# Performance work log

Hardware: AMD Instinct MI355X
Metric: run time of the kernel (lower is better)

The kernel has to match this reference:

```python
import jax, jax.numpy as jnp
import numpy as np

O_FEATURES = 4096
I_FEATURES = 4096
N_TOKENS = 8192


def _unpack_int4(packed, out_shape):
    # packed: int32 holding uint8 byte values; two signed int4 per byte (offset-8)
    p = packed.astype(jnp.int32)
    even = (p & 15) - 8          # low nibble
    odd = ((p >> 4) & 15) - 8    # high nibble
    # interleave: stacked[0::2] = even, stacked[1::2] = odd
    stacked = jnp.stack([even, odd], axis=-1).reshape(-1)
    return stacked.reshape(out_shape)


def setup_inputs() -> dict:
    key = jax.random.key(0)
    k1, k2, k3 = jax.random.split(key, 3)
    x = jax.random.normal(k1, (N_TOKENS, I_FEATURES), dtype=jnp.float32)
    packed_w = jax.random.randint(k2, (O_FEATURES * I_FEATURES // 2,), 0, 256, dtype=jnp.int32)
    # per-output-channel scale (positive, as produced by abs-max / qmax)
    scale = jax.random.uniform(k3, (O_FEATURES, 1), dtype=jnp.float32) * 0.01 + 1e-4
    return {"x": x, "packed_w": packed_w, "scale": scale}


def reference(x, packed_w, scale):
    # dequantize: unpack int4 -> target dtype, multiply per-row scale
    int_w = _unpack_int4(packed_w, (O_FEATURES, I_FEATURES)).astype(x.dtype)  # [O, I]
    w = int_w * scale.astype(x.dtype)  # scale broadcasts [O,1] over [O,I]
    # downstream quantized linear: y = x @ W^T
    return jnp.einsum('ni,oi->no', x, w)
```

## Files before the change

kernel.cpp:

```cpp
#include <hip/hip_runtime.h>

typedef unsigned char u8;
typedef signed char s8;
typedef unsigned int u32;
typedef __attribute__((ext_vector_type(4))) int i32x4;

#define M_TOK 8192
#define N_OUT 4096
#define K_IN  4096
#define NT    32

static __device__ __forceinline__ u32 pack4(float4 v, float inv) {
    int q0 = __float2int_rn(v.x * inv) & 255;
    int q1 = __float2int_rn(v.y * inv) & 255;
    int q2 = __float2int_rn(v.z * inv) & 255;
    int q3 = __float2int_rn(v.w * inv) & 255;
    return (u32)q0 | ((u32)q1 << 8) | ((u32)q2 << 16) | ((u32)q3 << 24);
}

__global__ __launch_bounds__(256) void quant_x_kernel(const float* __restrict__ x,
                                                      s8* __restrict__ xq,
                                                      float* __restrict__ sx) {
    int row = blockIdx.x;
    int t = threadIdx.x;
    const float4* xr = (const float4*)(x + (size_t)row * K_IN);
    float4 v0 = xr[t], v1 = xr[t + 256], v2 = xr[t + 512], v3 = xr[t + 768];
    float am = 0.f;
    am = fmaxf(am, fmaxf(fmaxf(fabsf(v0.x), fabsf(v0.y)), fmaxf(fabsf(v0.z), fabsf(v0.w))));
    am = fmaxf(am, fmaxf(fmaxf(fabsf(v1.x), fabsf(v1.y)), fmaxf(fabsf(v1.z), fabsf(v1.w))));
    am = fmaxf(am, fmaxf(fmaxf(fabsf(v2.x), fabsf(v2.y)), fmaxf(fabsf(v2.z), fabsf(v2.w))));
    am = fmaxf(am, fmaxf(fmaxf(fabsf(v3.x), fabsf(v3.y)), fmaxf(fabsf(v3.z), fabsf(v3.w))));
#pragma unroll
    for (int o = 32; o > 0; o >>= 1) am = fmaxf(am, __shfl_xor(am, o));
    __shared__ float red[4];
    if ((t & 63) == 0) red[t >> 6] = am;
    __syncthreads();
    am = fmaxf(fmaxf(red[0], red[1]), fmaxf(red[2], red[3]));
    float inv = (am > 0.f) ? 127.f / am : 0.f;
    if (t == 0) sx[row] = (am > 0.f) ? am / 127.f : 0.f;
    u32* out = (u32*)(xq + (size_t)row * K_IN);
    out[t]       = pack4(v0, inv);
    out[t + 256] = pack4(v1, inv);
    out[t + 512] = pack4(v2, inv);
    out[t + 768] = pack4(v3, inv);
}

__global__ __launch_bounds__(256) void unpack_w_kernel(const int* __restrict__ pw,
                                                       s8* __restrict__ wq, int n4) {
    int idx = blockIdx.x * blockDim.x + threadIdx.x;
    int stride = gridDim.x * blockDim.x;
    for (int i = idx; i < n4; i += stride) {
        int4 p = *(const int4*)(pw + (size_t)i * 4);
        u32 lo = (u32)(((p.x & 15) - 8) & 255)
               | ((u32)((((p.x >> 4) & 15) - 8) & 255) << 8)
               | ((u32)((((p.y) & 15) - 8) & 255) << 16)
               | ((u32)((((p.y >> 4) & 15) - 8) & 255) << 24);
        u32 hi = (u32)(((p.z & 15) - 8) & 255)
               | ((u32)((((p.z >> 4) & 15) - 8) & 255) << 8)
               | ((u32)((((p.w) & 15) - 8) & 255) << 16)
               | ((u32)((((p.w >> 4) & 15) - 8) & 255) << 24);
        uint2 o; o.x = lo; o.y = hi;
        *(uint2*)(wq + (size_t)i * 8) = o;
    }
}

#define MFMA(a, b, c) __builtin_amdgcn_mfma_i32_16x16x64_i8(a, b, c, 0, 0, 0)

static __device__ __forceinline__ i32x4 ldsv(const u8* p, int idx) {
    return *(const i32x4*)(p + idx);
}

#define MFMA16(A00, A01, A10, A11, M0, M1)                \
    acc[M0][0] = MFMA(A00, b00, acc[M0][0]);              \
    acc[M0][1] = MFMA(A00, b10, acc[M0][1]);              \
    acc[M0][2] = MFMA(A00, b20, acc[M0][2]);              \
    acc[M0][3] = MFMA(A00, b30, acc[M0][3]);              \
    acc[M1][0] = MFMA(A10, b00, acc[M1][0]);              \
    acc[M1][1] = MFMA(A10, b10, acc[M1][1]);              \
    acc[M1][2] = MFMA(A10, b20, acc[M1][2]);              \
    acc[M1][3] = MFMA(A10, b30, acc[M1][3]);              \
    acc[M0][0] = MFMA(A01, b01, acc[M0][0]);              \
    acc[M0][1] = MFMA(A01, b11, acc[M0][1]);              \
    acc[M0][2] = MFMA(A01, b21, acc[M0][2]);              \
    acc[M0][3] = MFMA(A01, b31, acc[M0][3]);              \
    acc[M1][0] = MFMA(A11, b01, acc[M1][0]);              \
    acc[M1][1] = MFMA(A11, b11, acc[M1][1]);              \
    acc[M1][2] = MFMA(A11, b21, acc[M1][2]);              \
    acc[M1][3] = MFMA(A11, b31, acc[M1][3]);

__global__ __launch_bounds__(512, 2) void gemm8p_i8_kernel(const s8* __restrict__ A,
                                                           const s8* __restrict__ B,
                                                           const float* __restrict__ sx,
                                                           const float* __restrict__ scale,
                                                           float* __restrict__ C) {
    __shared__ __align__(16) u8 lds[131072];

#define GLo(src, dstIdx)                                                        \
    __builtin_amdgcn_global_load_lds(                                           \
        (const __attribute__((address_space(1))) void*)(src),                   \
        (__attribute__((address_space(3))) void*)&lds[dstIdx], 16, 0, 0)

    int wg = blockIdx.x;
    int swz = (wg & 7) * 64 + (wg >> 3);
    int bm = swz >> 4;
    int bn = swz & 15;

    int t = threadIdx.x;
    int l = t & 63;
    int wid = t >> 6;
    int wr = wid >> 2;
    int wc = wid & 3;

    const size_t soff = (size_t)(t >> 3) * K_IN + (size_t)((((t & 7) ^ ((t >> 3) & 7)) << 4));
    const size_t S64 = (size_t)64 * K_IN;
    const int t16 = t * 16;

    const s8* Alo = A + (size_t)(bm * 256) * K_IN;
    const s8* Ahi = Alo + (size_t)128 * K_IN;
    const s8* Blo = B + (size_t)(bn * 256) * K_IN;
    const s8* Bhi = Blo + (size_t)128 * K_IN;

    const int kx = (l & 7) << 4;
    const int koff0 = (((l >> 4) << 4)) ^ kx;
    const int koff1 = koff0 ^ 64;
    const int aB = wr * 16384 + (l & 15) * 128;
    const int bB = 32768 + wc * 8192 + (l & 15) * 128;

    i32x4 acc[8][4] = {};

    GLo(Blo + soff, 32768 + t16);         GLo(Blo + soff + S64, 32768 + t16 + 8192);
    GLo(Bhi + soff, 49152 + t16);         GLo(Bhi + soff + S64, 49152 + t16 + 8192);
    GLo(Alo + soff, t16);                 GLo(Alo + soff + S64, t16 + 8192);
    GLo(Ahi + soff, 16384 + t16);         GLo(Ahi + soff + S64, 16384 + t16 + 8192);
    GLo(Blo + soff + 128, 98304 + t16);   GLo(Blo + soff + S64 + 128, 98304 + t16 + 8192);
    GLo(Bhi + soff + 128, 114688 + t16);  GLo(Bhi + soff + S64 + 128, 114688 + t16 + 8192);
    asm volatile("s_waitcnt vmcnt(4)" ::: "memory");
    __builtin_amdgcn_s_barrier();

    for (int T = 0; T < NT; ++T) {
        const int buf = T & 1;
        const u8* L = lds + buf * 65536;

        i32x4 b00 = ldsv(L, bB + koff0),        b01 = ldsv(L, bB + koff1);
        i32x4 b10 = ldsv(L, bB + 2048 + koff0), b11 = ldsv(L, bB + 2048 + koff1);
        i32x4 b20 = ldsv(L, bB + 4096 + koff0), b21 = ldsv(L, bB + 4096 + koff1);
        i32x4 b30 = ldsv(L, bB + 6144 + koff0), b31 = ldsv(L, bB + 6144 + koff1);
        i32x4 a00 = ldsv(L, aB + koff0),        a01 = ldsv(L, aB + koff1);
        i32x4 a10 = ldsv(L, aB + 2048 + koff0), a11 = ldsv(L, aB + 2048 + koff1);
        if (T + 1 < NT) {
            size_t ko = (size_t)(T + 1) * 128;
            int d = (buf ^ 1) * 65536 + t16;
            GLo(Alo + soff + ko, d);                 GLo(Alo + soff + S64 + ko, d + 8192);
            GLo(Ahi + soff + ko, d + 16384);         GLo(Ahi + soff + S64 + ko, d + 24576);
        }
        __builtin_amdgcn_s_barrier();
        asm volatile("s_waitcnt lgkmcnt(0)" ::: "memory");
        __builtin_amdgcn_s_setprio(1);
        MFMA16(a00, a01, a10, a11, 0, 1);
        __builtin_amdgcn_s_setprio(0);
        __builtin_amdgcn_s_barrier();

        a00 = ldsv(L, aB + 4096 + koff0); a01 = ldsv(L, aB + 4096 + koff1);
        a10 = ldsv(L, aB + 6144 + koff0); a11 = ldsv(L, aB + 6144 + koff1);
        if (T + 2 < NT) {
            size_t ko = (size_t)(T + 2) * 128;
            int d = buf * 65536 + 32768 + t16;
            GLo(Blo + soff + ko, d);  GLo(Blo + soff + S64 + ko, d + 8192);
        }
        __builtin_amdgcn_s_barrier();
        asm volatile("s_waitcnt lgkmcnt(0)" ::: "memory");
        __builtin_amdgcn_s_setprio(1);
        MFMA16(a00, a01, a10, a11, 2, 3);
        __builtin_amdgcn_s_setprio(0);
        __builtin_amdgcn_s_barrier();

        a00 = ldsv(L, aB + 8192 + koff0);  a01 = ldsv(L, aB + 8192 + koff1);
        a10 = ldsv(L, aB + 10240 + koff0); a11 = ldsv(L, aB + 10240 + koff1);
        if (T + 2 < NT) {
            size_t ko = (size_t)(T + 2) * 128;
            int d = buf * 65536 + 49152 + t16;
            GLo(Bhi + soff + ko, d);  GLo(Bhi + soff + S64 + ko, d + 8192);
        }
        __builtin_amdgcn_s_barrier();
        asm volatile("s_waitcnt lgkmcnt(0)" ::: "memory");
        __builtin_amdgcn_s_setprio(1);
        MFMA16(a00, a01, a10, a11, 4, 5);
        __builtin_amdgcn_s_setprio(0);
        __builtin_amdgcn_s_barrier();

        a00 = ldsv(L, aB + 12288 + koff0); a01 = ldsv(L, aB + 12288 + koff1);
        a10 = ldsv(L, aB + 14336 + koff0); a11 = ldsv(L, aB + 14336 + koff1);
        __builtin_amdgcn_s_barrier();
        asm volatile("s_waitcnt lgkmcnt(0)" ::: "memory");
        __builtin_amdgcn_s_setprio(1);
        MFMA16(a00, a01, a10, a11, 6, 7);
        __builtin_amdgcn_s_setprio(0);
        if (T < NT - 2) asm volatile("s_waitcnt vmcnt(4)" ::: "memory");
        else            asm volatile("s_waitcnt vmcnt(0)" ::: "memory");
        __builtin_amdgcn_s_barrier();
    }

    int col0 = bn * 256 + wc * 64 + (l & 15);
    float sc_[4];
#pragma unroll
    for (int n = 0; n < 4; ++n) sc_[n] = scale[col0 + n * 16];

#pragma unroll
    for (int m = 0; m < 8; ++m) {
        int row0 = bm * 256 + wr * 128 + m * 16 + (l >> 4) * 4;
        float4 sxr = *(const float4*)(sx + row0);
        float sxa[4] = {sxr.x, sxr.y, sxr.z, sxr.w};
#pragma unroll
        for (int n = 0; n < 4; ++n) {
            int gcol = col0 + n * 16;
#pragma unroll
            for (int j = 0; j < 4; ++j)
                C[(size_t)(row0 + j) * N_OUT + gcol] = (float)acc[m][n][j] * sxa[j] * sc_[n];
        }
    }
#undef GLo
}

__global__ __launch_bounds__(256) void gemm_fb_kernel(const float* __restrict__ X,
                                                      const int* __restrict__ PW,
                                                      const float* __restrict__ S,
                                                      float* __restrict__ C) {
    __shared__ float sxm[64][33];
    __shared__ float swm[64][33];
    int bm = blockIdx.x / (N_OUT / 64);
    int bn = blockIdx.x % (N_OUT / 64);
    int t = threadIdx.x;
    int r = t >> 2, c8 = (t & 3) * 8;
    int tx = t & 15, ty = t >> 4;
    float acc[4][4] = {};
    for (int k0 = 0; k0 < K_IN; k0 += 32) {
        const float* xs = X + (size_t)(bm * 64 + r) * K_IN + k0 + c8;
#pragma unroll
        for (int j = 0; j < 8; ++j) sxm[r][c8 + j] = xs[j];
        const int* ps = PW + ((size_t)(bn * 64 + r) * K_IN + k0 + c8) / 2;
#pragma unroll
        for (int j = 0; j < 4; ++j) {
            int b = ps[j];
            swm[r][c8 + 2 * j]     = (float)((b & 15) - 8);
            swm[r][c8 + 2 * j + 1] = (float)(((b >> 4) & 15) - 8);
        }
        __syncthreads();
#pragma unroll
        for (int kk = 0; kk < 32; ++kk) {
            float a[4], w[4];
#pragma unroll
            for (int i = 0; i < 4; ++i) a[i] = sxm[ty * 4 + i][kk];
#pragma unroll
            for (int j = 0; j < 4; ++j) w[j] = swm[tx * 4 + j][kk];
#pragma unroll
            for (int i = 0; i < 4; ++i)
#pragma unroll
                for (int j = 0; j < 4; ++j) acc[i][j] += a[i] * w[j];
        }
        __syncthreads();
    }
#pragma unroll
    for (int i = 0; i < 4; ++i) {
        int gr = bm * 64 + ty * 4 + i;
#pragma unroll
        for (int j = 0; j < 4; ++j) {
            int gc = bn * 64 + tx * 4 + j;
            C[(size_t)gr * N_OUT + gc] = acc[i][j] * S[gc];
        }
    }
}

extern "C" void kernel_launch(void* const* d_in, const int* in_sizes, int n_in,
                              void* d_out, int out_size, void* d_ws, size_t ws_size,
                              hipStream_t stream) {
    const float* x  = (const float*)d_in[0];
    const int*   pw = (const int*)d_in[1];
    const float* sc = (const float*)d_in[2];
    float* out = (float*)d_out;

    const size_t xq_bytes = (size_t)M_TOK * K_IN;
    const size_t wq_bytes = (size_t)N_OUT * K_IN;
    const size_t sx_bytes = (size_t)M_TOK * sizeof(float);
    const size_t need = xq_bytes + wq_bytes + sx_bytes;

    if (ws_size >= need) {
        s8* xq = (s8*)d_ws;
        s8* wq = xq + xq_bytes;
        float* sx = (float*)(wq + wq_bytes);
        quant_x_kernel<<<dim3(M_TOK), dim3(256), 0, stream>>>(x, xq, sx);
        unpack_w_kernel<<<dim3(2048), dim3(256), 0, stream>>>(pw, wq,
                                                              (int)(((size_t)N_OUT * K_IN / 2) / 4));
        gemm8p_i8_kernel<<<dim3((M_TOK / 256) * (N_OUT / 256)), dim3(512), 0, stream>>>(
            xq, wq, sx, sc, out);
    } else {
        gemm_fb_kernel<<<dim3((M_TOK / 64) * (N_OUT / 64)), dim3(256), 0, stream>>>(x, pw, sc, out);
    }
}
```

Before: 170.6 us.

## Fuse prep kernels and cut GEMM inner loop from four phases to two

The activation quantization and weight unpack kernels are merged into one launch. Extra blocks handle the unpack, which saves a kernel launch and lets the two run concurrently. The GEMM main loop now loads twice as many A fragments per phase and issues 32 MFMAs per barrier pair instead of 16, halving the barriers per K-step. Both B-half prefetches are also issued together. The trade-off is more live registers under launch_bounds(512,2), which could spill, and fewer points where loads can interleave with compute.

New measurement: 176.0 us, median of 5. 1.03x slower.

```diff
diff --git a/kernel.cpp b/kernel.cpp
--- a/kernel.cpp
+++ b/kernel.cpp
@@ -18,49 +18,52 @@
     return (u32)q0 | ((u32)q1 << 8) | ((u32)q2 << 16) | ((u32)q3 << 24);
 }
 
-__global__ __launch_bounds__(256) void quant_x_kernel(const float* __restrict__ x,
-                                                      s8* __restrict__ xq,
-                                                      float* __restrict__ sx) {
-    int row = blockIdx.x;
+__global__ __launch_bounds__(256) void prep_kernel(const float* __restrict__ x,
+                                                   const int* __restrict__ pw,
+                                                   s8* __restrict__ xq,
+                                                   float* __restrict__ sx,
+                                                   s8* __restrict__ wq) {
+    __shared__ float red[4];
+    int bid = blockIdx.x;
     int t = threadIdx.x;
-    const float4* xr = (const float4*)(x + (size_t)row * K_IN);
-    float4 v0 = xr[t], v1 = xr[t + 256], v2 = xr[t + 512], v3 = xr[t + 768];
-    float am = 0.f;
-    am = fmaxf(am, fmaxf(fmaxf(fabsf(v0.x), fabsf(v0.y)), fmaxf(fabsf(v0.z), fabsf(v0.w))));
-    am = fmaxf(am, fmaxf(fmaxf(fabsf(v1.x), fabsf(v1.y)), fmaxf(fabsf(v1.z), fabsf(v1.w))));
-    am = fmaxf(am, fmaxf(fmaxf(fabsf(v2.x), fabsf(v2.y)), fmaxf(fabsf(v2.z), fabsf(v2.w))));
-    am = fmaxf(am, fmaxf(fmaxf(fabsf(v3.x), fabsf(v3.y)), fmaxf(fabsf(v3.z), fabsf(v3.w))));
-#pragma unroll
-    for (int o = 32; o > 0; o >>= 1) am = fmaxf(am, __shfl_xor(am, o));
-    __shared__ float red[4];
-    if ((t & 63) == 0) red[t >> 6] = am;
-    __syncthreads();
-    am = fmaxf(fmaxf(red[0], red[1]), fmaxf(red[2], red[3]));
-    float inv = (am > 0.f) ? 127.f / am : 0.f;
-    if (t == 0) sx[row] = (am > 0.f) ? am / 127.f : 0.f;
-    u32* out = (u32*)(xq + (size_t)row * K_IN);
-    out[t]       = pack4(v0, inv);
-    out[t + 256] = pack4(v1, inv);
-    out[t + 512] = pack4(v2, inv);
-    out[t + 768] = pack4(v3, inv);
-}
-
-__global__ __launch_bounds__(256) void unpack_w_kernel(const int* __restrict__ pw,
-                                                       s8* __restrict__ wq, int n4) {
-    int idx = blockIdx.x * blockDim.x + threadIdx.x;
-    int stride = gridDim.x * blockDim.x;
-    for (int i = idx; i < n4; i += stride) {
-        int4 p = *(const int4*)(pw + (size_t)i * 4);
-        u32 lo = (u32)(((p.x & 15) - 8) & 255)
-               | ((u32)((((p.x >> 4) & 15) - 8) & 255) << 8)
-               | ((u32)((((p.y) & 15) - 8) & 255) << 16)
-               | ((u32)((((p.y >> 4) & 15) - 8) & 255) << 24);
-        u32 hi = (u32)(((p.z & 15) - 8) & 255)
-               | ((u32)((((p.z >> 4) & 15) - 8) & 255) << 8)
-               | ((u32)((((p.w) & 15) - 8) & 255) << 16)
-               | ((u32)((((p.w >> 4) & 15) - 8) & 255) << 24);
-        uint2 o; o.x = lo; o.y = hi;
-        *(uint2*)(wq + (size_t)i * 8) = o;
+    if (bid < M_TOK) {
+        int row = bid;
+        const float4* xr = (const float4*)(x + (size_t)row * K_IN);
+        float4 v0 = xr[t], v1 = xr[t + 256], v2 = xr[t + 512], v3 = xr[t + 768];
+        float am = 0.f;
+        am = fmaxf(am, fmaxf(fmaxf(fabsf(v0.x), fabsf(v0.y)), fmaxf(fabsf(v0.z), fabsf(v0.w))));
+        am = fmaxf(am, fmaxf(fmaxf(fabsf(v1.x), fabsf(v1.y)), fmaxf(fabsf(v1.z), fabsf(v1.w))));
+        am = fmaxf(am, fmaxf(fmaxf(fabsf(v2.x), fabsf(v2.y)), fmaxf(fabsf(v2.z), fabsf(v2.w))));
+        am = fmaxf(am, fmaxf(fmaxf(fabsf(v3.x), fabsf(v3.y)), fmaxf(fabsf(v3.z), fabsf(v3.w))));
+#pragma unroll
+        for (int o = 32; o > 0; o >>= 1) am = fmaxf(am, __shfl_xor(am, o));
+        if ((t & 63) == 0) red[t >> 6] = am;
+        __syncthreads();
+        am = fmaxf(fmaxf(red[0], red[1]), fmaxf(red[2], red[3]));
+        float inv = (am > 0.f) ? 127.f / am : 0.f;
+        if (t == 0) sx[row] = (am > 0.f) ? am / 127.f : 0.f;
+        u32* out = (u32*)(xq + (size_t)row * K_IN);
+        out[t]       = pack4(v0, inv);
+        out[t + 256] = pack4(v1, inv);
+        out[t + 512] = pack4(v2, inv);
+        out[t + 768] = pack4(v3, inv);
+    } else {
+        const int n4 = (N_OUT * K_IN / 2) / 4;
+        int idx = (bid - M_TOK) * 256 + t;
+        const int stride = 512 * 256;
+        for (int i = idx; i < n4; i += stride) {
+            int4 p = *(const int4*)(pw + (size_t)i * 4);
+            u32 lo = (u32)(((p.x & 15) - 8) & 255)
+                   | ((u32)((((p.x >> 4) & 15) - 8) & 255) << 8)
+                   | ((u32)((((p.y) & 15) - 8) & 255) << 16)
+                   | ((u32)((((p.y >> 4) & 15) - 8) & 255) << 24);
+            u32 hi = (u32)(((p.z & 15) - 8) & 255)
+                   | ((u32)((((p.z >> 4) & 15) - 8) & 255) << 8)
+                   | ((u32)((((p.w) & 15) - 8) & 255) << 16)
+                   | ((u32)((((p.w >> 4) & 15) - 8) & 255) << 24);
+            uint2 o; o.x = lo; o.y = hi;
+            *(uint2*)(wq + (size_t)i * 8) = o;
+        }
     }
 }
 
@@ -88,7 +91,7 @@
     acc[M1][2] = MFMA(A11, b21, acc[M1][2]);              \
     acc[M1][3] = MFMA(A11, b31, acc[M1][3]);
 
-__global__ __launch_bounds__(512, 2) void gemm8p_i8_kernel(const s8* __restrict__ A,
+__global__ __launch_bounds__(512, 2) void gemm2p_i8_kernel(const s8* __restrict__ A,
                                                            const s8* __restrict__ B,
                                                            const float* __restrict__ sx,
                                                            const float* __restrict__ scale,
@@ -147,6 +150,8 @@
         i32x4 b30 = ldsv(L, bB + 6144 + koff0), b31 = ldsv(L, bB + 6144 + koff1);
         i32x4 a00 = ldsv(L, aB + koff0),        a01 = ldsv(L, aB + koff1);
         i32x4 a10 = ldsv(L, aB + 2048 + koff0), a11 = ldsv(L, aB + 2048 + koff1);
+        i32x4 a20 = ldsv(L, aB + 4096 + koff0), a21 = ldsv(L, aB + 4096 + koff1);
+        i32x4 a30 = ldsv(L, aB + 6144 + koff0), a31 = ldsv(L, aB + 6144 + koff1);
         if (T + 1 < NT) {
             size_t ko = (size_t)(T + 1) * 128;
             int d = (buf ^ 1) * 65536 + t16;
@@ -157,43 +162,25 @@
         asm volatile("s_waitcnt lgkmcnt(0)" ::: "memory");
         __builtin_amdgcn_s_setprio(1);
         MFMA16(a00, a01, a10, a11, 0, 1);
+        MFMA16(a20, a21, a30, a31, 2, 3);
         __builtin_amdgcn_s_setprio(0);
         __builtin_amdgcn_s_barrier();
 
-        a00 = ldsv(L, aB + 4096 + koff0); a01 = ldsv(L, aB + 4096 + koff1);
-        a10 = ldsv(L, aB + 6144 + koff0); a11 = ldsv(L, aB + 6144 + koff1);
+        a00 = ldsv(L, aB + 8192 + koff0);  a01 = ldsv(L, aB + 8192 + koff1);
+        a10 = ldsv(L, aB + 10240 + koff0); a11 = ldsv(L, aB + 10240 + koff1);
+        a20 = ldsv(L, aB + 12288 + koff0); a21 = ldsv(L, aB + 12288 + koff1);
+        a30 = ldsv(L, aB + 14336 + koff0); a31 = ldsv(L, aB + 14336 + koff1);
         if (T + 2 < NT) {
             size_t ko = (size_t)(T + 2) * 128;
             int d = buf * 65536 + 32768 + t16;
             GLo(Blo + soff + ko, d);  GLo(Blo + soff + S64 + ko, d + 8192);
-        }
-        __builtin_amdgcn_s_barrier();
-        asm volatile("s_waitcnt lgkmcnt(0)" ::: "memory");
-        __builtin_amdgcn_s_setprio(1);
-        MFMA16(a00, a01, a10, a11, 2, 3);
-        __builtin_amdgcn_s_setprio(0);
-        __builtin_amdgcn_s_barrier();
-
-        a00 = ldsv(L, aB + 8192 + koff0);  a01 = ldsv(L, aB + 8192 + koff1);
-        a10 = ldsv(L, aB + 10240 + koff0); a11 = ldsv(L, aB + 10240 + koff1);
-        if (T + 2 < NT) {
-            size_t ko = (size_t)(T + 2) * 128;
-            int d = buf * 65536 + 49152 + t16;
-            GLo(Bhi + soff + ko, d);  GLo(Bhi + soff + S64 + ko, d + 8192);
+            GLo(Bhi + soff + ko, d + 16384);  GLo(Bhi + soff + S64 + ko, d + 24576);
         }
         __builtin_amdgcn_s_barrier();
         asm volatile("s_waitcnt lgkmcnt(0)" ::: "memory");
         __builtin_amdgcn_s_setprio(1);
         MFMA16(a00, a01, a10, a11, 4, 5);
-        __builtin_amdgcn_s_setprio(0);
-        __builtin_amdgcn_s_barrier();
-
-        a00 = ldsv(L, aB + 12288 + koff0); a01 = ldsv(L, aB + 12288 + koff1);
-        a10 = ldsv(L, aB + 14336 + koff0); a11 = ldsv(L, aB + 14336 + koff1);
-        __builtin_amdgcn_s_barrier();
-        asm volatile("s_waitcnt lgkmcnt(0)" ::: "memory");
-        __builtin_amdgcn_s_setprio(1);
-        MFMA16(a00, a01, a10, a11, 6, 7);
+        MFMA16(a20, a21, a30, a31, 6, 7);
         __builtin_amdgcn_s_setprio(0);
         if (T < NT - 2) asm volatile("s_waitcnt vmcnt(4)" ::: "memory");
         else            asm volatile("s_waitcnt vmcnt(0)" ::: "memory");
@@ -287,10 +274,8 @@
         s8* xq = (s8*)d_ws;
         s8* wq = xq + xq_bytes;
         float* sx = (float*)(wq + wq_bytes);
-        quant_x_kernel<<<dim3(M_TOK), dim3(256), 0, stream>>>(x, xq, sx);
-        unpack_w_kernel<<<dim3(2048), dim3(256), 0, stream>>>(pw, wq,
-                                                              (int)(((size_t)N_OUT * K_IN / 2) / 4));
-        gemm8p_i8_kernel<<<dim3((M_TOK / 256) * (N_OUT / 256)), dim3(512), 0, stream>>>(
+        prep_kernel<<<dim3(M_TOK + 512), dim3(256), 0, stream>>>(x, pw, xq, sx, wq);
+        gemm2p_i8_kernel<<<dim3((M_TOK / 256) * (N_OUT / 256)), dim3(512), 0, stream>>>(
             xq, wq, sx, sc, out);
     } else {
         gemm_fb_kernel<<<dim3((M_TOK / 64) * (N_OUT / 64)), dim3(256), 0, stream>>>(x, pw, sc, out);
```
